# Optimization experiments

Hardware: AMD Instinct MI355X
Metric: run time of the kernel (lower is better)

## Reference

```python
import jax, jax.numpy as jnp
import numpy as np

THRESH = 0.5   # global `thresh` used by ActFun
LENS = 0.5     # global `lens` (surrogate width)
DECAY = 0.25   # LIFNode init_decay
INV_STD = 1.0 / float(np.sqrt(1.0 + 1e-5))  # BN eval: running_mean=0, running_var=1
HEADS = 8
WINDOW = 8

@jax.custom_vjp
def act_fun(x):
    return (x > THRESH).astype(x.dtype)

def _act_fwd(x):
    return act_fun(x), x

def _act_bwd(x, g):
    temp = (jnp.abs(x - THRESH) < LENS).astype(g.dtype) / (2.0 * LENS)
    return (g * temp,)

act_fun.defvjp(_act_fwd, _act_bwd)

def lif(x):
    # x: [T, ...]; mem = x[0]; mem_t = mem_{t-1}*decay*(1-spike_{t-1}.detach()) + x_t
    spike0 = act_fun(x[0])
    def step(carry, xi):
        mem_prev, spike_prev = carry
        mem = mem_prev * DECAY * (1.0 - jax.lax.stop_gradient(spike_prev)) + xi
        spike = act_fun(mem)
        return (mem, spike), spike
    _, spikes = jax.lax.scan(step, (x[0], spike0), x[1:])
    return jnp.concatenate([spike0[None], spikes], axis=0)

def bn_eval(x, gamma, beta):
    # BatchNorm2d eval over channel D (last dim of [T,B,L,D]) with default running stats
    return x * (INV_STD * gamma) + beta

def linear(x, w, b):
    # torch nn.Linear: y = x @ w.T + b, w: [out, in]
    return jnp.einsum('tbld,ed->tble', x, w) + b


def setup_inputs() -> dict:
    key = jax.random.key(0)
    ks = jax.random.split(key, 12)
    T, B, L, D = 4, 4, 1024, 512
    s = 0.02
    inp = {
        'x': jax.random.normal(ks[0], (T, B, L, D), dtype=jnp.float32),
        'pos_bias': jax.random.uniform(ks[1], (L, L), dtype=jnp.float32),
        'q_w': jax.random.normal(ks[2], (D, D), dtype=jnp.float32) * s,
        'q_b': jnp.zeros((D,), jnp.float32),
        'q_g': jnp.ones((D,), jnp.float32),
        'q_beta': jnp.zeros((D,), jnp.float32),
        'k_w': jax.random.normal(ks[3], (D, D), dtype=jnp.float32) * s,
        'k_b': jnp.zeros((D,), jnp.float32),
        'k_g': jnp.ones((D,), jnp.float32),
        'k_beta': jnp.zeros((D,), jnp.float32),
        'v_w': jax.random.normal(ks[4], (D, D), dtype=jnp.float32) * s,
        'v_b': jnp.zeros((D,), jnp.float32),
        'v_g': jnp.ones((D,), jnp.float32),
        'v_beta': jnp.zeros((D,), jnp.float32),
        'last_w': jax.random.normal(ks[5], (D, D), dtype=jnp.float32) * s,
        'last_b': jnp.zeros((D,), jnp.float32),
        'last_g': jnp.ones((D,), jnp.float32),
        'last_beta': jnp.zeros((D,), jnp.float32),
    }
    return inp


def reference(x, pos_bias, q_w, q_b, q_g, q_beta, k_w, k_b, k_g, k_beta,
              v_w, v_b, v_g, v_beta, last_w, last_b, last_g, last_beta):
    T, B, L, D = x.shape
    H = HEADS
    Dh = D // H
    # local causal band: keep pos_bias[i,j] only where 0 <= i-j < WINDOW
    i = jnp.arange(L)[:, None]
    j = jnp.arange(L)[None, :]
    band = ((i - j) >= 0) & ((i - j) < WINDOW)
    pb = jnp.where(band, pos_bias[:L, :L], 0.0)  # [L, L]

    xs = lif(x)  # first_lif
    q = lif(bn_eval(linear(xs, q_w, q_b), q_g, q_beta))
    k = lif(bn_eval(linear(xs, k_w, k_b), k_g, k_beta))
    v = lif(bn_eval(linear(xs, v_w, v_b), v_g, v_beta))

    # [T,B,L,D] -> [T,B,L,H,Dh] -> [B,H,L,T,Dh] -> [B,H,L,T*Dh]
    qh = q.reshape(T, B, L, H, Dh).transpose(1, 3, 2, 0, 4).reshape(B, H, L, T * Dh)
    kv = (k * v).reshape(T, B, L, H, Dh).transpose(1, 3, 2, 0, 4).reshape(B, H, L, T * Dh)

    attn = jnp.einsum('ij,bhjd->bhid', pb, kv)  # local-window positional mixing
    out = qh * attn
    out = out.reshape(B, H, L, T, Dh).transpose(3, 0, 2, 1, 4).reshape(T, B, L, D)
    out = lif(out)  # attn_lif
    out = bn_eval(linear(out, last_w, last_b), last_g, last_beta)
    return out
```

## Files before the change

### kernel.cpp

```cpp
#include <hip/hip_runtime.h>
#include <stdint.h>


#define T_ 4
#define B_ 4
#define L_ 1024
#define D_ 512
#define BI_ (B_*L_)
#define M_ROWS (T_*B_*L_)
#define STRIDE4 (B_*L_*D_/4)
#define INV_STD 0.9999950000374997f
#define EPS_FLAG 1e-3f
#define LIST_CAP 5000000u

typedef unsigned int   u32;
typedef unsigned short u16;
typedef __bf16 bf16x8 __attribute__((ext_vector_type(8)));
typedef float  f32x4  __attribute__((ext_vector_type(4)));

static __device__ __forceinline__ float spike_of(float m) {
  return m > 0.5f ? 1.0f : 0.0f;
}
static __device__ __forceinline__ u16 sbits(float s) {
  return s != 0.0f ? (u16)0x3F80 : (u16)0;
}

__device__ __forceinline__ void gll16(const u16* g, void* l) {
  __builtin_amdgcn_global_load_lds(
      (const __attribute__((address_space(1))) u32*)(const void*)g,
      (__attribute__((address_space(3))) u32*)l, 16, 0, 0);
}

__global__ __launch_bounds__(256) void k_wsplit(const float* __restrict__ qw,
    const float* __restrict__ kw, const float* __restrict__ vw,
    const float* __restrict__ lw, u16* __restrict__ wsp, u32* __restrict__ cnt) {
  int idx = blockIdx.x * 256 + threadIdx.x;
  if (idx == 0) *cnt = 0;
  int mat = idx >> 16;
  int u = idx & 65535;
  const float* W = mat == 0 ? qw : mat == 1 ? kw : mat == 2 ? vw : lw;
  float4 w = ((const float4*)W)[u];
  float wv[4] = {w.x, w.y, w.z, w.w};
  u16 hb[4], lb[4];
#pragma unroll
  for (int c = 0; c < 4; ++c) {
    __bf16 h = (__bf16)wv[c];
    float r = wv[c] - (float)h;
    __bf16 lo = (__bf16)r;
    hb[c] = __builtin_bit_cast(u16, h);
    lb[c] = __builtin_bit_cast(u16, lo);
  }
  u16* base = wsp + (size_t)mat * 524288;
  ((ushort4*)base)[u]            = make_ushort4(hb[0], hb[1], hb[2], hb[3]);
  ((ushort4*)(base + 262144))[u] = make_ushort4(lb[0], lb[1], lb[2], lb[3]);
}

__global__ __launch_bounds__(256) void k_lif_first(const float* __restrict__ x,
                                                   u16* __restrict__ xsb) {
  int idx = blockIdx.x * 256 + threadIdx.x;
  if (idx >= STRIDE4) return;
  const int bi = idx >> 7, d4 = idx & 127;
  const float4* x4 = (const float4*)x;
  ushort4* o4 = (ushort4*)xsb;
  float m[4], s[4];
  float4 v = x4[idx];
  m[0] = v.x; m[1] = v.y; m[2] = v.z; m[3] = v.w;
#pragma unroll
  for (int c = 0; c < 4; ++c) s[c] = spike_of(m[c]);
  o4[(bi * 4 + 0) * 128 + d4] =
      make_ushort4(sbits(s[0]), sbits(s[1]), sbits(s[2]), sbits(s[3]));
#pragma unroll
  for (int t = 1; t < T_; ++t) {
    v = x4[idx + t * STRIDE4];
    float xv[4] = {v.x, v.y, v.z, v.w};
#pragma unroll
    for (int c = 0; c < 4; ++c) {
      m[c] = m[c] * 0.25f * (1.0f - s[c]) + xv[c];
      s[c] = spike_of(m[c]);
    }
    o4[(bi * 4 + t) * 128 + d4] =
        make_ushort4(sbits(s[0]), sbits(s[1]), sbits(s[2]), sbits(s[3]));
  }
}

__device__ __forceinline__ void gemm_core(const u16* __restrict__ Ab,
    const u16* __restrict__ Wp, int row0, int col0, int tid,
    unsigned char* sm, f32x4 (&acc)[4][4]) {
  const u16* gsrc[12];
  int loff[12];
#pragma unroll
  for (int u = 0; u < 12; ++u) {
    if (u < 4) {
      int lin = u * 4096 + tid * 16;
      int r = lin >> 7, slot = (lin >> 4) & 7, gs = slot ^ (r & 7);
      gsrc[u] = Ab + (size_t)(row0 + r) * 512 + gs * 8;
      loff[u] = lin;
    } else {
      int lin = (u - 4) * 4096 + tid * 16;
      int plane = lin >> 14, l3 = lin & 16383;
      int r = l3 >> 7, slot = (l3 >> 4) & 7, gs = slot ^ (r & 7);
      gsrc[u] = Wp + (size_t)plane * 262144 + (size_t)(col0 + r) * 512 + gs * 8;
      loff[u] = 16384 + lin;
    }
  }
  const int lane = tid & 63;
  const int wid = tid >> 6;
  const int wr = wid >> 1, wc = wid & 1;
  const int la = lane & 15, lg = lane >> 4;

  int offA[4][2], offB[2][4][2];
#pragma unroll
  for (int mi = 0; mi < 4; ++mi) {
    int r = wr * 64 + mi * 16 + la;
#pragma unroll
    for (int s = 0; s < 2; ++s)
      offA[mi][s] = r * 128 + ((s * 64 + lg * 16) ^ ((r & 7) << 4));
  }
#pragma unroll
  for (int p = 0; p < 2; ++p)
#pragma unroll
    for (int ni = 0; ni < 4; ++ni) {
      int r = wc * 64 + ni * 16 + la;
#pragma unroll
      for (int s = 0; s < 2; ++s)
        offB[p][ni][s] = 16384 + p * 16384 + r * 128 +
                         ((s * 64 + lg * 16) ^ ((r & 7) << 4));
    }

#pragma unroll
  for (int a = 0; a < 4; ++a)
#pragma unroll
    for (int b = 0; b < 4; ++b) acc[a][b] = (f32x4){0.f, 0.f, 0.f, 0.f};

  for (int k0 = 0; k0 < 8; ++k0) {
#pragma unroll
    for (int u = 0; u < 12; ++u) gll16(gsrc[u] + (k0 << 6), sm + loff[u]);
    __syncthreads();
    uint4 af[4][2];
#pragma unroll
    for (int mi = 0; mi < 4; ++mi)
#pragma unroll
      for (int s = 0; s < 2; ++s)
        af[mi][s] = *(const uint4*)(sm + offA[mi][s]);
#pragma unroll
    for (int p = 0; p < 2; ++p)
#pragma unroll
      for (int s = 0; s < 2; ++s)
#pragma unroll
        for (int ni = 0; ni < 4; ++ni) {
          uint4 bf = *(const uint4*)(sm + offB[p][ni][s]);
#pragma unroll
          for (int mi = 0; mi < 4; ++mi)
            acc[mi][ni] = __builtin_amdgcn_mfma_f32_16x16x32_bf16(
                __builtin_bit_cast(bf16x8, af[mi][s]),
                __builtin_bit_cast(bf16x8, bf), acc[mi][ni], 0, 0, 0);
        }
    __syncthreads();
  }
}

__global__ __launch_bounds__(256) void k_gemm_qkv(const u16* __restrict__ Ab,
    const u16* __restrict__ wsp,
    const float* __restrict__ qb2, const float* __restrict__ qg,
    const float* __restrict__ qbe,
    const float* __restrict__ kb2, const float* __restrict__ kg,
    const float* __restrict__ kbe,
    const float* __restrict__ vb2, const float* __restrict__ vg,
    const float* __restrict__ vbe,
    u16* __restrict__ qs, u16* __restrict__ ks, u16* __restrict__ vs,
    u32* __restrict__ list, u32* __restrict__ cnt) {
  __shared__ __align__(16) unsigned char sm[49152];
  const int tid = threadIdx.x;
  const int tz = blockIdx.z;
  const u16* Wp = wsp + (size_t)tz * 524288;
  const float* Bb = tz == 0 ? qb2 : tz == 1 ? kb2 : vb2;
  const float* Gg = tz == 0 ? qg  : tz == 1 ? kg  : vg;
  const float* Be = tz == 0 ? qbe : tz == 1 ? kbe : vbe;
  u16* S          = tz == 0 ? qs  : tz == 1 ? ks  : vs;

  int f = blockIdx.y * 4 + blockIdx.x;
  int tI = (f & 7) * 64 + (f >> 3);
  const int row0 = (tI >> 2) * 128;
  const int col0 = (tI & 3) * 128;

  f32x4 acc[4][4];
  gemm_core(Ab, Wp, row0, col0, tid, sm, acc);

  const int lane = tid & 63;
  const int wid = tid >> 6;
  const int wr = wid >> 1, wc = wid & 1;
  const int la = lane & 15, lg = lane >> 4;

  u16* sm16 = (u16*)sm;
#pragma unroll
  for (int ni = 0; ni < 4; ++ni) {
    int cl = wc * 64 + ni * 16 + la;
    int e = col0 + cl;
    float cs = INV_STD * Gg[e];
    float cb = Bb[e], ct = Be[e];
#pragma unroll
    for (int mi = 0; mi < 4; ++mi) {
      int rl = wr * 64 + mi * 16 + lg * 4;
      int bi = (row0 + rl) >> 2;
      float m = 0.f, s = 0.f;
      int fl = 0;
#pragma unroll
      for (int p = 0; p < 4; ++p) {
        float pre = (acc[mi][ni][p] + cb) * cs + ct;
        if (p == 0) m = pre;
        else m = m * 0.25f * (1.0f - s) + pre;
        s = spike_of(m);
        if (fabsf(m - 0.5f) < EPS_FLAG) fl = 1;
        sm16[(rl + p) * 128 + cl] = sbits(s);
      }
      if (fl) {
        u32 pos = atomicAdd(cnt, 1u);
        if (pos < LIST_CAP)
          list[pos] = ((u32)tz << 21) | (u32)(bi * 512 + e);
      }
    }
  }
  __syncthreads();
#pragma unroll
  for (int ps = 0; ps < 8; ++ps) {
    int rr = ps * 16 + (tid >> 4);
    int c8 = (tid & 15) * 8;
    uint4 vv = *(const uint4*)(sm16 + rr * 128 + c8);
    *(uint4*)(S + (size_t)(row0 + rr) * 512 + col0 + c8) = vv;
  }
}

__global__ __launch_bounds__(256) void k_gemm_out(const u16* __restrict__ Ab,
    const u16* __restrict__ Wp, const float* __restrict__ bias,
    const float* __restrict__ gamma, const float* __restrict__ beta,
    float* __restrict__ Y) {
  __shared__ __align__(16) unsigned char sm[49152];
  const int tid = threadIdx.x;
  int f = blockIdx.y * 4 + blockIdx.x;
  int tI = (f & 7) * 64 + (f >> 3);
  const int row0 = (tI >> 2) * 128;
  const int col0 = (tI & 3) * 128;

  f32x4 acc[4][4];
  gemm_core(Ab, Wp, row0, col0, tid, sm, acc);

  const int lane = tid & 63;
  const int wid = tid >> 6;
  const int wr = wid >> 1, wc = wid & 1;
  const int la = lane & 15, lg = lane >> 4;

  float* sm32 = (float*)sm;
#pragma unroll
  for (int h = 0; h < 2; ++h) {
    if (wr == h) {
#pragma unroll
      for (int ni = 0; ni < 4; ++ni) {
        int cl = wc * 64 + ni * 16 + la;
        int e = col0 + cl;
        float cs = INV_STD * gamma[e];
        float cb = bias[e], ct = beta[e];
#pragma unroll
        for (int mi = 0; mi < 4; ++mi) {
          int rb = mi * 16 + lg * 4;
#pragma unroll
          for (int p = 0; p < 4; ++p)
            sm32[(rb + p) * 128 + cl] = (acc[mi][ni][p] + cb) * cs + ct;
        }
      }
    }
    __syncthreads();
    int rl = tid >> 2;
    int q0 = (tid & 3) * 32;
    int gr = row0 + h * 64 + rl;
    int bi = gr >> 2, p = gr & 3;
    float* dst = Y + ((size_t)p * BI_ + bi) * 512 + col0 + q0;
    const float* srcl = sm32 + rl * 128 + q0;
#pragma unroll
    for (int u = 0; u < 8; ++u)
      ((uint4*)dst)[u] = ((const uint4*)srcl)[u];
    __syncthreads();
  }
}

__device__ __forceinline__ void consume32_1(const float4 (&wb)[8],
                                            const uint4 (&ab)[4], float& c) {
#pragma unroll
  for (int u = 0; u < 8; ++u) {
    float4 w = wb[u];
    uint4 tt = ab[u >> 1];
    u32 a = (u & 1) ? tt.z : tt.x, b = (u & 1) ? tt.w : tt.y;
    c += (a & 0xFFFFu) ? w.x : 0.0f;
    c += (a >> 16)     ? w.y : 0.0f;
    c += (b & 0xFFFFu) ? w.z : 0.0f;
    c += (b >> 16)     ? w.w : 0.0f;
  }
}

__global__ __launch_bounds__(128) void k_fixup_c(const u16* __restrict__ xsb,
    u16* __restrict__ qs, u16* __restrict__ ks, u16* __restrict__ vs,
    const float* __restrict__ qw, const float* __restrict__ qb2,
    const float* __restrict__ qg, const float* __restrict__ qbe,
    const float* __restrict__ kw, const float* __restrict__ kb2,
    const float* __restrict__ kg, const float* __restrict__ kbe,
    const float* __restrict__ vw, const float* __restrict__ vb2,
    const float* __restrict__ vg, const float* __restrict__ vbe,
    const u32* __restrict__ list, const u32* __restrict__ cnt) {
  u32 n = *cnt;
  if (n > LIST_CAP) n = LIST_CAP;
  u32 tot = n * 4;
  for (u32 ii = blockIdx.x * 128 + threadIdx.x; ii < tot;
       ii += gridDim.x * 128) {
    u32 i = ii >> 2;
    int t = (int)(ii & 3);
    u32 e = list[i];
    int tz = (int)(e >> 21);
    int col = (int)(e & 0x1FFFFFu);
    int bi = col >> 9, d = col & 511;
    const float* W  = tz == 0 ? qw  : tz == 1 ? kw  : vw;
    const float* Bb = tz == 0 ? qb2 : tz == 1 ? kb2 : vb2;
    const float* Gg = tz == 0 ? qg  : tz == 1 ? kg  : vg;
    const float* Be = tz == 0 ? qbe : tz == 1 ? kbe : vbe;
    u16* S          = tz == 0 ? qs  : tz == 1 ? ks  : vs;
    const float4* w4 = (const float4*)(W + (size_t)d * 512);
    const uint4*  R  = (const uint4*)(xsb + ((size_t)bi * 4 + t) * 512);

    float4 wA[8], wB[8];
    uint4 aA[4], aB[4];
#pragma unroll
    for (int u = 0; u < 8; ++u) wA[u] = w4[u];
#pragma unroll
    for (int u = 0; u < 4; ++u) aA[u] = R[u];
    float c = 0.f;
#pragma unroll
    for (int ch = 0; ch < 16; ++ch) {
      if ((ch & 1) == 0) {
        if (ch + 1 < 16) {
          int wb0 = (ch + 1) * 8, ab0 = (ch + 1) * 4;
#pragma unroll
          for (int u = 0; u < 8; ++u) wB[u] = w4[wb0 + u];
#pragma unroll
          for (int u = 0; u < 4; ++u) aB[u] = R[ab0 + u];
        }
        consume32_1(wA, aA, c);
      } else {
        if (ch + 1 < 16) {
          int wb0 = (ch + 1) * 8, ab0 = (ch + 1) * 4;
#pragma unroll
          for (int u = 0; u < 8; ++u) wA[u] = w4[wb0 + u];
#pragma unroll
          for (int u = 0; u < 4; ++u) aA[u] = R[ab0 + u];
        }
        consume32_1(wB, aB, c);
      }
    }
    int lane = threadIdx.x & 63;
    int qb = lane & ~3;
    float cq[4];
    cq[0] = __shfl(c, qb + 0, 64);
    cq[1] = __shfl(c, qb + 1, 64);
    cq[2] = __shfl(c, qb + 2, 64);
    cq[3] = __shfl(c, qb + 3, 64);
    float cs = INV_STD * Gg[d];
    float cb = Bb[d], ct = Be[d];
    float m = 0.f, s = 0.f;
    u16 myb = 0;
#pragma unroll
    for (int t2 = 0; t2 < 4; ++t2) {
      float pre = (cq[t2] + cb) * cs + ct;
      if (t2 == 0) m = pre;
      else m = m * 0.25f * (1.0f - s) + pre;
      s = spike_of(m);
      if (t2 == t) myb = sbits(s);
    }
    S[((size_t)bi * 4 + t) * 512 + d] = myb;
  }
}

__global__ __launch_bounds__(256) void k_attn(const u16* __restrict__ qs,
    const u16* __restrict__ ks, const u16* __restrict__ vs,
    const float* __restrict__ pos_bias, u16* __restrict__ sout) {
  int idx = blockIdx.x * 256 + threadIdx.x;
  if (idx >= STRIDE4) return;
  const int d4 = idx & 127;
  const int bi = idx >> 7;
  const int i = bi & (L_ - 1);
  const int wmax = i < 7 ? i : 7;

  float pbv[8];
  const float* pbrow = pos_bias + (size_t)i * L_ + i;
  for (int w = 0; w <= wmax; ++w) pbv[w] = pbrow[-w];

  const ushort4* k4 = (const ushort4*)ks;
  const ushort4* v4 = (const ushort4*)vs;
  const ushort4* q4 = (const ushort4*)qs;
  float pre[T_][4];

#pragma unroll
  for (int t = 0; t < T_; ++t) {
    float sum[4] = {0.f, 0.f, 0.f, 0.f};
    for (int w = wmax; w >= 0; --w) {
      int rj = ((bi - w) * 4 + t) * 128 + d4;
      ushort4 ku = k4[rj];
      ushort4 vu = v4[rj];
      sum[0] += (ku.x && vu.x) ? pbv[w] : 0.0f;
      sum[1] += (ku.y && vu.y) ? pbv[w] : 0.0f;
      sum[2] += (ku.z && vu.z) ? pbv[w] : 0.0f;
      sum[3] += (ku.w && vu.w) ? pbv[w] : 0.0f;
    }
    ushort4 qu = q4[(bi * 4 + t) * 128 + d4];
    pre[t][0] = qu.x ? sum[0] : 0.0f;
    pre[t][1] = qu.y ? sum[1] : 0.0f;
    pre[t][2] = qu.z ? sum[2] : 0.0f;
    pre[t][3] = qu.w ? sum[3] : 0.0f;
  }

  ushort4* s4 = (ushort4*)sout;
  float m[4], s[4];
#pragma unroll
  for (int c = 0; c < 4; ++c) { m[c] = pre[0][c]; s[c] = spike_of(m[c]); }
  s4[(bi * 4 + 0) * 128 + d4] =
      make_ushort4(sbits(s[0]), sbits(s[1]), sbits(s[2]), sbits(s[3]));
#pragma unroll
  for (int t = 1; t < T_; ++t) {
#pragma unroll
    for (int c = 0; c < 4; ++c) {
      m[c] = m[c] * 0.25f * (1.0f - s[c]) + pre[t][c];
      s[c] = spike_of(m[c]);
    }
    s4[(bi * 4 + t) * 128 + d4] =
        make_ushort4(sbits(s[0]), sbits(s[1]), sbits(s[2]), sbits(s[3]));
  }
}

extern "C" void kernel_launch(void* const* d_in, const int* in_sizes, int n_in,
                              void* d_out, int out_size, void* d_ws, size_t ws_size,
                              hipStream_t stream) {
  (void)in_sizes; (void)n_in; (void)out_size; (void)ws_size;
  const float* x        = (const float*)d_in[0];
  const float* pos_bias = (const float*)d_in[1];
  const float* q_w    = (const float*)d_in[2];
  const float* q_b    = (const float*)d_in[3];
  const float* q_g    = (const float*)d_in[4];
  const float* q_beta = (const float*)d_in[5];
  const float* k_w    = (const float*)d_in[6];
  const float* k_b    = (const float*)d_in[7];
  const float* k_g    = (const float*)d_in[8];
  const float* k_beta = (const float*)d_in[9];
  const float* v_w    = (const float*)d_in[10];
  const float* v_b    = (const float*)d_in[11];
  const float* v_g    = (const float*)d_in[12];
  const float* v_beta = (const float*)d_in[13];
  const float* last_w    = (const float*)d_in[14];
  const float* last_b    = (const float*)d_in[15];
  const float* last_g    = (const float*)d_in[16];
  const float* last_beta = (const float*)d_in[17];
  float* out = (float*)d_out;

  char* ws = (char*)d_ws;
  u16*   xsb  = (u16*)(ws + 0);
  u16*   qs   = (u16*)(ws + 16777216);
  u16*   ks   = (u16*)(ws + 33554432);
  u16*   vs   = (u16*)(ws + 50331648);
  u16*   sA   = (u16*)(ws + 67108864);
  u16*   wsp  = (u16*)(ws + 100663296);
  u32*   list = (u32*)(ws + 104857600);
  u32*   cnt  = (u32*)(ws + 124857600);

  k_wsplit<<<1024, 256, 0, stream>>>(q_w, k_w, v_w, last_w, wsp, cnt);
  k_lif_first<<<2048, 256, 0, stream>>>(x, xsb);

  dim3 gq(4, 128, 3);
  k_gemm_qkv<<<gq, 256, 0, stream>>>(xsb, wsp,
      q_b, q_g, q_beta, k_b, k_g, k_beta, v_b, v_g, v_beta,
      qs, ks, vs, list, cnt);

  k_fixup_c<<<2048, 128, 0, stream>>>(xsb, qs, ks, vs,
      q_w, q_b, q_g, q_beta, k_w, k_b, k_g, k_beta, v_w, v_b, v_g, v_beta,
      list, cnt);

  k_attn<<<2048, 256, 0, stream>>>(qs, ks, vs, pos_bias, sA);

  dim3 gg(4, 128);
  k_gemm_out<<<gg, 256, 0, stream>>>(sA, wsp + 3 * 524288,
                                     last_b, last_g, last_beta, out);
}
```

Measured before the change: 348.6 us.

## Double-buffer GEMM K-tiles in LDS to overlap global loads with MFMA

```diff
diff --git a/kernel.cpp b/kernel.cpp
--- a/kernel.cpp
+++ b/kernel.cpp
@@ -86,45 +86,41 @@
 __device__ __forceinline__ void gemm_core(const u16* __restrict__ Ab,
     const u16* __restrict__ Wp, int row0, int col0, int tid,
     unsigned char* sm, f32x4 (&acc)[4][4]) {
-  const u16* gsrc[12];
-  int loff[12];
-#pragma unroll
-  for (int u = 0; u < 12; ++u) {
-    if (u < 4) {
-      int lin = u * 4096 + tid * 16;
-      int r = lin >> 7, slot = (lin >> 4) & 7, gs = slot ^ (r & 7);
-      gsrc[u] = Ab + (size_t)(row0 + r) * 512 + gs * 8;
-      loff[u] = lin;
-    } else {
-      int lin = (u - 4) * 4096 + tid * 16;
-      int plane = lin >> 14, l3 = lin & 16383;
-      int r = l3 >> 7, slot = (l3 >> 4) & 7, gs = slot ^ (r & 7);
-      gsrc[u] = Wp + (size_t)plane * 262144 + (size_t)(col0 + r) * 512 + gs * 8;
-      loff[u] = 16384 + lin;
-    }
-  }
   const int lane = tid & 63;
   const int wid = tid >> 6;
   const int wr = wid >> 1, wc = wid & 1;
   const int la = lane & 15, lg = lane >> 4;
 
-  int offA[4][2], offB[2][4][2];
+  const u16* gA[2]; int lA[2];
+#pragma unroll
+  for (int u = 0; u < 2; ++u) {
+    int lin = u * 4096 + tid * 16;
+    int r = lin >> 6, slot = (lin >> 4) & 3, gs = slot ^ (r & 3);
+    gA[u] = Ab + (size_t)(row0 + r) * 512 + gs * 8;
+    lA[u] = lin;
+  }
+  const u16* gB[4]; int lB[4];
+#pragma unroll
+  for (int u = 0; u < 4; ++u) {
+    int lin = u * 4096 + tid * 16;
+    int plane = lin >> 13, l2 = lin & 8191;
+    int r = l2 >> 6, slot = (l2 >> 4) & 3, gs = slot ^ (r & 3);
+    gB[u] = Wp + (size_t)plane * 262144 + (size_t)(col0 + r) * 512 + gs * 8;
+    lB[u] = 8192 + lin;
+  }
+
+  int offA[4], offB[2][4];
 #pragma unroll
   for (int mi = 0; mi < 4; ++mi) {
     int r = wr * 64 + mi * 16 + la;
-#pragma unroll
-    for (int s = 0; s < 2; ++s)
-      offA[mi][s] = r * 128 + ((s * 64 + lg * 16) ^ ((r & 7) << 4));
+    offA[mi] = r * 64 + ((lg ^ (r & 3)) << 4);
   }
 #pragma unroll
   for (int p = 0; p < 2; ++p)
 #pragma unroll
     for (int ni = 0; ni < 4; ++ni) {
       int r = wc * 64 + ni * 16 + la;
-#pragma unroll
-      for (int s = 0; s < 2; ++s)
-        offB[p][ni][s] = 16384 + p * 16384 + r * 128 +
-                         ((s * 64 + lg * 16) ^ ((r & 7) << 4));
+      offB[p][ni] = 8192 + p * 8192 + r * 64 + ((lg ^ (r & 3)) << 4);
     }
 
 #pragma unroll
@@ -132,29 +128,38 @@
 #pragma unroll
     for (int b = 0; b < 4; ++b) acc[a][b] = (f32x4){0.f, 0.f, 0.f, 0.f};
 
-  for (int k0 = 0; k0 < 8; ++k0) {
-#pragma unroll
-    for (int u = 0; u < 12; ++u) gll16(gsrc[u] + (k0 << 6), sm + loff[u]);
-    __syncthreads();
-    uint4 af[4][2];
-#pragma unroll
-    for (int mi = 0; mi < 4; ++mi)
-#pragma unroll
-      for (int s = 0; s < 2; ++s)
-        af[mi][s] = *(const uint4*)(sm + offA[mi][s]);
+#pragma unroll
+  for (int u = 0; u < 2; ++u) gll16(gA[u], sm + lA[u]);
+#pragma unroll
+  for (int u = 0; u < 4; ++u) gll16(gB[u], sm + lB[u]);
+  __syncthreads();
+
+#pragma unroll 2
+  for (int t = 0; t < 16; ++t) {
+    const int cur = t & 1;
+    const int nb = (cur ^ 1) * 24576;
+    if (t < 15) {
+      const int ko = (t + 1) * 32;
+#pragma unroll
+      for (int u = 0; u < 2; ++u) gll16(gA[u] + ko, sm + nb + lA[u]);
+#pragma unroll
+      for (int u = 0; u < 4; ++u) gll16(gB[u] + ko, sm + nb + lB[u]);
+    }
+    const unsigned char* bb = sm + cur * 24576;
+    uint4 af[4];
+#pragma unroll
+    for (int mi = 0; mi < 4; ++mi) af[mi] = *(const uint4*)(bb + offA[mi]);
 #pragma unroll
     for (int p = 0; p < 2; ++p)
 #pragma unroll
-      for (int s = 0; s < 2; ++s)
-#pragma unroll
-        for (int ni = 0; ni < 4; ++ni) {
-          uint4 bf = *(const uint4*)(sm + offB[p][ni][s]);
-#pragma unroll
-          for (int mi = 0; mi < 4; ++mi)
-            acc[mi][ni] = __builtin_amdgcn_mfma_f32_16x16x32_bf16(
-                __builtin_bit_cast(bf16x8, af[mi][s]),
-                __builtin_bit_cast(bf16x8, bf), acc[mi][ni], 0, 0, 0);
-        }
+      for (int ni = 0; ni < 4; ++ni) {
+        uint4 bf = *(const uint4*)(bb + offB[p][ni]);
+#pragma unroll
+        for (int mi = 0; mi < 4; ++mi)
+          acc[mi][ni] = __builtin_amdgcn_mfma_f32_16x16x32_bf16(
+              __builtin_bit_cast(bf16x8, af[mi]),
+              __builtin_bit_cast(bf16x8, bf), acc[mi][ni], 0, 0, 0);
+      }
     __syncthreads();
   }
 }
```

Result: no change. 355.5 us (+2.0%).

## Switch spike GEMMs to int8 MFMA with two-level per-row weight quantization

Applied to the files above, without the earlier changes.

```diff
diff --git a/kernel.cpp b/kernel.cpp
--- a/kernel.cpp
+++ b/kernel.cpp
@@ -7,68 +7,82 @@
 #define L_ 1024
 #define D_ 512
 #define BI_ (B_*L_)
-#define M_ROWS (T_*B_*L_)
 #define STRIDE4 (B_*L_*D_/4)
 #define INV_STD 0.9999950000374997f
 #define EPS_FLAG 1e-3f
 #define LIST_CAP 5000000u
 
 typedef unsigned int   u32;
-typedef unsigned short u16;
-typedef __bf16 bf16x8 __attribute__((ext_vector_type(8)));
-typedef float  f32x4  __attribute__((ext_vector_type(4)));
+typedef unsigned char  u8;
+typedef int i32x4 __attribute__((ext_vector_type(4)));
 
 static __device__ __forceinline__ float spike_of(float m) {
   return m > 0.5f ? 1.0f : 0.0f;
 }
-static __device__ __forceinline__ u16 sbits(float s) {
-  return s != 0.0f ? (u16)0x3F80 : (u16)0;
-}
-
-__device__ __forceinline__ void gll16(const u16* g, void* l) {
+
+__device__ __forceinline__ void gll16(const void* g, void* l) {
   __builtin_amdgcn_global_load_lds(
-      (const __attribute__((address_space(1))) u32*)(const void*)g,
+      (const __attribute__((address_space(1))) u32*)g,
       (__attribute__((address_space(3))) u32*)l, 16, 0, 0);
 }
 
 __global__ __launch_bounds__(256) void k_wsplit(const float* __restrict__ qw,
     const float* __restrict__ kw, const float* __restrict__ vw,
-    const float* __restrict__ lw, u16* __restrict__ wsp, u32* __restrict__ cnt) {
-  int idx = blockIdx.x * 256 + threadIdx.x;
-  if (idx == 0) *cnt = 0;
-  int mat = idx >> 16;
-  int u = idx & 65535;
+    const float* __restrict__ lw, u8* __restrict__ Wq,
+    float* __restrict__ scl, u32* __restrict__ cnt) {
+  if (blockIdx.x == 0 && threadIdx.x == 0) *cnt = 0;
+  int gid = blockIdx.x * 4 + (threadIdx.x >> 6);
+  int mat = gid >> 9, e = gid & 511;
+  int lane = threadIdx.x & 63;
   const float* W = mat == 0 ? qw : mat == 1 ? kw : mat == 2 ? vw : lw;
-  float4 w = ((const float4*)W)[u];
-  float wv[4] = {w.x, w.y, w.z, w.w};
-  u16 hb[4], lb[4];
-#pragma unroll
-  for (int c = 0; c < 4; ++c) {
-    __bf16 h = (__bf16)wv[c];
-    float r = wv[c] - (float)h;
-    __bf16 lo = (__bf16)r;
-    hb[c] = __builtin_bit_cast(u16, h);
-    lb[c] = __builtin_bit_cast(u16, lo);
-  }
-  u16* base = wsp + (size_t)mat * 524288;
-  ((ushort4*)base)[u]            = make_ushort4(hb[0], hb[1], hb[2], hb[3]);
-  ((ushort4*)(base + 262144))[u] = make_ushort4(lb[0], lb[1], lb[2], lb[3]);
+  const float4* w4 = (const float4*)(W + (size_t)e * 512 + lane * 8);
+  float4 wa = w4[0], wb = w4[1];
+  float w[8] = {wa.x, wa.y, wa.z, wa.w, wb.x, wb.y, wb.z, wb.w};
+  float am = 0.f;
+#pragma unroll
+  for (int j = 0; j < 8; ++j) am = fmaxf(am, fabsf(w[j]));
+#pragma unroll
+  for (int off = 1; off < 64; off <<= 1)
+    am = fmaxf(am, __shfl_xor(am, off, 64));
+  float s1 = am > 0.f ? am * (1.0f / 127.0f) : 1.0f;
+  float s2 = s1 * (1.0f / 254.0f);
+  float inv1 = 1.0f / s1, inv2 = 1.0f / s2;
+  u32 p1lo = 0, p1hi = 0, p2lo = 0, p2hi = 0;
+#pragma unroll
+  for (int j = 0; j < 8; ++j) {
+    float q1 = rintf(w[j] * inv1);
+    q1 = fminf(127.f, fmaxf(-127.f, q1));
+    float r = w[j] - s1 * q1;
+    float q2 = rintf(r * inv2);
+    q2 = fminf(127.f, fmaxf(-127.f, q2));
+    u32 b1 = (u32)(u8)(signed char)(int)q1;
+    u32 b2 = (u32)(u8)(signed char)(int)q2;
+    if (j < 4) { p1lo |= b1 << (j * 8); p2lo |= b2 << (j * 8); }
+    else       { p1hi |= b1 << ((j - 4) * 8); p2hi |= b2 << ((j - 4) * 8); }
+  }
+  u8* base = Wq + (size_t)mat * 524288 + (size_t)e * 512 + lane * 8;
+  *(uint2*)base             = make_uint2(p1lo, p1hi);
+  *(uint2*)(base + 262144)  = make_uint2(p2lo, p2hi);
+  if (lane == 0) {
+    scl[mat * 1024 + e] = s1;
+    scl[mat * 1024 + 512 + e] = s2;
+  }
 }
 
 __global__ __launch_bounds__(256) void k_lif_first(const float* __restrict__ x,
-                                                   u16* __restrict__ xsb) {
+                                                   u8* __restrict__ xsb) {
   int idx = blockIdx.x * 256 + threadIdx.x;
   if (idx >= STRIDE4) return;
   const int bi = idx >> 7, d4 = idx & 127;
   const float4* x4 = (const float4*)x;
-  ushort4* o4 = (ushort4*)xsb;
+  uchar4* o4 = (uchar4*)xsb;
   float m[4], s[4];
   float4 v = x4[idx];
   m[0] = v.x; m[1] = v.y; m[2] = v.z; m[3] = v.w;
 #pragma unroll
   for (int c = 0; c < 4; ++c) s[c] = spike_of(m[c]);
   o4[(bi * 4 + 0) * 128 + d4] =
-      make_ushort4(sbits(s[0]), sbits(s[1]), sbits(s[2]), sbits(s[3]));
+      make_uchar4((u8)s[0], (u8)s[1], (u8)s[2], (u8)s[3]);
 #pragma unroll
   for (int t = 1; t < T_; ++t) {
     v = x4[idx + t * STRIDE4];
@@ -79,27 +93,27 @@
       s[c] = spike_of(m[c]);
     }
     o4[(bi * 4 + t) * 128 + d4] =
-        make_ushort4(sbits(s[0]), sbits(s[1]), sbits(s[2]), sbits(s[3]));
-  }
-}
-
-__device__ __forceinline__ void gemm_core(const u16* __restrict__ Ab,
-    const u16* __restrict__ Wp, int row0, int col0, int tid,
-    unsigned char* sm, f32x4 (&acc)[4][4]) {
-  const u16* gsrc[12];
+        make_uchar4((u8)s[0], (u8)s[1], (u8)s[2], (u8)s[3]);
+  }
+}
+
+__device__ __forceinline__ void gemm_core_i8(const u8* __restrict__ Ab,
+    const u8* __restrict__ Wq2, int row0, int col0, int tid,
+    unsigned char* sm, i32x4 (&acc0)[4][4], i32x4 (&acc1)[4][4]) {
+  const u8* gsrc[12];
   int loff[12];
 #pragma unroll
   for (int u = 0; u < 12; ++u) {
     if (u < 4) {
       int lin = u * 4096 + tid * 16;
       int r = lin >> 7, slot = (lin >> 4) & 7, gs = slot ^ (r & 7);
-      gsrc[u] = Ab + (size_t)(row0 + r) * 512 + gs * 8;
+      gsrc[u] = Ab + (size_t)(row0 + r) * 512 + gs * 16;
       loff[u] = lin;
     } else {
       int lin = (u - 4) * 4096 + tid * 16;
       int plane = lin >> 14, l3 = lin & 16383;
       int r = l3 >> 7, slot = (l3 >> 4) & 7, gs = slot ^ (r & 7);
-      gsrc[u] = Wp + (size_t)plane * 262144 + (size_t)(col0 + r) * 512 + gs * 8;
+      gsrc[u] = Wq2 + (size_t)plane * 262144 + (size_t)(col0 + r) * 512 + gs * 16;
       loff[u] = 16384 + lin;
     }
   }
@@ -113,8 +127,8 @@
   for (int mi = 0; mi < 4; ++mi) {
     int r = wr * 64 + mi * 16 + la;
 #pragma unroll
-    for (int s = 0; s < 2; ++s)
-      offA[mi][s] = r * 128 + ((s * 64 + lg * 16) ^ ((r & 7) << 4));
+    for (int ks = 0; ks < 2; ++ks)
+      offA[mi][ks] = r * 128 + (((ks * 4 + lg) ^ (r & 7)) << 4);
   }
 #pragma unroll
   for (int p = 0; p < 2; ++p)
@@ -122,80 +136,94 @@
     for (int ni = 0; ni < 4; ++ni) {
       int r = wc * 64 + ni * 16 + la;
 #pragma unroll
-      for (int s = 0; s < 2; ++s)
-        offB[p][ni][s] = 16384 + p * 16384 + r * 128 +
-                         ((s * 64 + lg * 16) ^ ((r & 7) << 4));
+      for (int ks = 0; ks < 2; ++ks)
+        offB[p][ni][ks] = 16384 + p * 16384 + r * 128 +
+                          (((ks * 4 + lg) ^ (r & 7)) << 4);
     }
 
 #pragma unroll
   for (int a = 0; a < 4; ++a)
 #pragma unroll
-    for (int b = 0; b < 4; ++b) acc[a][b] = (f32x4){0.f, 0.f, 0.f, 0.f};
-
-  for (int k0 = 0; k0 < 8; ++k0) {
-#pragma unroll
-    for (int u = 0; u < 12; ++u) gll16(gsrc[u] + (k0 << 6), sm + loff[u]);
+    for (int b = 0; b < 4; ++b) {
+      acc0[a][b] = (i32x4){0, 0, 0, 0};
+      acc1[a][b] = (i32x4){0, 0, 0, 0};
+    }
+
+  for (int k0 = 0; k0 < 4; ++k0) {
+#pragma unroll
+    for (int u = 0; u < 12; ++u) gll16(gsrc[u] + (k0 << 7), sm + loff[u]);
     __syncthreads();
     uint4 af[4][2];
 #pragma unroll
     for (int mi = 0; mi < 4; ++mi)
 #pragma unroll
-      for (int s = 0; s < 2; ++s)
-        af[mi][s] = *(const uint4*)(sm + offA[mi][s]);
-#pragma unroll
-    for (int p = 0; p < 2; ++p)
-#pragma unroll
-      for (int s = 0; s < 2; ++s)
-#pragma unroll
-        for (int ni = 0; ni < 4; ++ni) {
-          uint4 bf = *(const uint4*)(sm + offB[p][ni][s]);
-#pragma unroll
-          for (int mi = 0; mi < 4; ++mi)
-            acc[mi][ni] = __builtin_amdgcn_mfma_f32_16x16x32_bf16(
-                __builtin_bit_cast(bf16x8, af[mi][s]),
-                __builtin_bit_cast(bf16x8, bf), acc[mi][ni], 0, 0, 0);
-        }
+      for (int ks = 0; ks < 2; ++ks)
+        af[mi][ks] = *(const uint4*)(sm + offA[mi][ks]);
+#pragma unroll
+    for (int ks = 0; ks < 2; ++ks)
+#pragma unroll
+      for (int ni = 0; ni < 4; ++ni) {
+        uint4 bf = *(const uint4*)(sm + offB[0][ni][ks]);
+#pragma unroll
+        for (int mi = 0; mi < 4; ++mi)
+          acc0[mi][ni] = __builtin_amdgcn_mfma_i32_16x16x64_i8(
+              __builtin_bit_cast(i32x4, af[mi][ks]),
+              __builtin_bit_cast(i32x4, bf), acc0[mi][ni], 0, 0, 0);
+      }
+#pragma unroll
+    for (int ks = 0; ks < 2; ++ks)
+#pragma unroll
+      for (int ni = 0; ni < 4; ++ni) {
+        uint4 bf = *(const uint4*)(sm + offB[1][ni][ks]);
+#pragma unroll
+        for (int mi = 0; mi < 4; ++mi)
+          acc1[mi][ni] = __builtin_amdgcn_mfma_i32_16x16x64_i8(
+              __builtin_bit_cast(i32x4, af[mi][ks]),
+              __builtin_bit_cast(i32x4, bf), acc1[mi][ni], 0, 0, 0);
+      }
     __syncthreads();
   }
 }
 
-__global__ __launch_bounds__(256) void k_gemm_qkv(const u16* __restrict__ Ab,
-    const u16* __restrict__ wsp,
+__global__ __launch_bounds__(256) void k_gemm_qkv(const u8* __restrict__ Ab,
+    const u8* __restrict__ Wq, const float* __restrict__ scl,
     const float* __restrict__ qb2, const float* __restrict__ qg,
     const float* __restrict__ qbe,
     const float* __restrict__ kb2, const float* __restrict__ kg,
     const float* __restrict__ kbe,
     const float* __restrict__ vb2, const float* __restrict__ vg,
     const float* __restrict__ vbe,
-    u16* __restrict__ qs, u16* __restrict__ ks, u16* __restrict__ vs,
+    u8* __restrict__ qs, u8* __restrict__ ks, u8* __restrict__ vs,
     u32* __restrict__ list, u32* __restrict__ cnt) {
   __shared__ __align__(16) unsigned char sm[49152];
   const int tid = threadIdx.x;
   const int tz = blockIdx.z;
-  const u16* Wp = wsp + (size_t)tz * 524288;
+  const u8* Wp = Wq + (size_t)tz * 524288;
   const float* Bb = tz == 0 ? qb2 : tz == 1 ? kb2 : vb2;
   const float* Gg = tz == 0 ? qg  : tz == 1 ? kg  : vg;
   const float* Be = tz == 0 ? qbe : tz == 1 ? kbe : vbe;
-  u16* S          = tz == 0 ? qs  : tz == 1 ? ks  : vs;
+  u8* S           = tz == 0 ? qs  : tz == 1 ? ks  : vs;
 
   int f = blockIdx.y * 4 + blockIdx.x;
   int tI = (f & 7) * 64 + (f >> 3);
   const int row0 = (tI >> 2) * 128;
   const int col0 = (tI & 3) * 128;
 
-  f32x4 acc[4][4];
-  gemm_core(Ab, Wp, row0, col0, tid, sm, acc);
+  i32x4 acc0[4][4], acc1[4][4];
+  gemm_core_i8(Ab, Wp, row0, col0, tid, sm, acc0, acc1);
 
   const int lane = tid & 63;
   const int wid = tid >> 6;
   const int wr = wid >> 1, wc = wid & 1;
   const int la = lane & 15, lg = lane >> 4;
 
-  u16* sm16 = (u16*)sm;
+  u8* sm8 = sm;
 #pragma unroll
   for (int ni = 0; ni < 4; ++ni) {
     int cl = wc * 64 + ni * 16 + la;
     int e = col0 + cl;
+    float s1 = scl[tz * 1024 + e];
+    float s2 = scl[tz * 1024 + 512 + e];
     float cs = INV_STD * Gg[e];
     float cb = Bb[e], ct = Be[e];
 #pragma unroll
@@ -206,12 +234,13 @@
       int fl = 0;
 #pragma unroll
       for (int p = 0; p < 4; ++p) {
-        float pre = (acc[mi][ni][p] + cb) * cs + ct;
+        float raw = s1 * (float)acc0[mi][ni][p] + s2 * (float)acc1[mi][ni][p];
+        float pre = (raw + cb) * cs + ct;
         if (p == 0) m = pre;
         else m = m * 0.25f * (1.0f - s) + pre;
         s = spike_of(m);
         if (fabsf(m - 0.5f) < EPS_FLAG) fl = 1;
-        sm16[(rl + p) * 128 + cl] = sbits(s);
+        sm8[(rl + p) * 128 + cl] = (u8)s;
       }
       if (fl) {
         u32 pos = atomicAdd(cnt, 1u);
@@ -222,18 +251,18 @@
   }
   __syncthreads();
 #pragma unroll
-  for (int ps = 0; ps < 8; ++ps) {
-    int rr = ps * 16 + (tid >> 4);
-    int c8 = (tid & 15) * 8;
-    uint4 vv = *(const uint4*)(sm16 + rr * 128 + c8);
-    *(uint4*)(S + (size_t)(row0 + rr) * 512 + col0 + c8) = vv;
-  }
-}
-
-__global__ __launch_bounds__(256) void k_gemm_out(const u16* __restrict__ Ab,
-    const u16* __restrict__ Wp, const float* __restrict__ bias,
-    const float* __restrict__ gamma, const float* __restrict__ beta,
-    float* __restrict__ Y) {
+  for (int ps = 0; ps < 4; ++ps) {
+    int rr = ps * 32 + (tid >> 3);
+    int c16 = (tid & 7) * 16;
+    uint4 vv = *(const uint4*)(sm8 + rr * 128 + c16);
+    *(uint4*)(S + (size_t)(row0 + rr) * 512 + col0 + c16) = vv;
+  }
+}
+
+__global__ __launch_bounds__(256) void k_gemm_out(const u8* __restrict__ Ab,
+    const u8* __restrict__ Wq, const float* __restrict__ scl,
+    const float* __restrict__ bias, const float* __restrict__ gamma,
+    const float* __restrict__ beta, float* __restrict__ Y) {
   __shared__ __align__(16) unsigned char sm[49152];
   const int tid = threadIdx.x;
   int f = blockIdx.y * 4 + blockIdx.x;
@@ -241,8 +270,8 @@
   const int row0 = (tI >> 2) * 128;
   const int col0 = (tI & 3) * 128;
 
-  f32x4 acc[4][4];
-  gemm_core(Ab, Wp, row0, col0, tid, sm, acc);
+  i32x4 acc0[4][4], acc1[4][4];
+  gemm_core_i8(Ab, Wq + 3 * 524288, row0, col0, tid, sm, acc0, acc1);
 
   const int lane = tid & 63;
   const int wid = tid >> 6;
@@ -257,14 +286,19 @@
       for (int ni = 0; ni < 4; ++ni) {
         int cl = wc * 64 + ni * 16 + la;
         int e = col0 + cl;
+        float s1 = scl[3 * 1024 + e];
+        float s2 = scl[3 * 1024 + 512 + e];
         float cs = INV_STD * gamma[e];
         float cb = bias[e], ct = beta[e];
 #pragma unroll
         for (int mi = 0; mi < 4; ++mi) {
           int rb = mi * 16 + lg * 4;
 #pragma unroll
-          for (int p = 0; p < 4; ++p)
-            sm32[(rb + p) * 128 + cl] = (acc[mi][ni][p] + cb) * cs + ct;
+          for (int p = 0; p < 4; ++p) {
+            float raw = s1 * (float)acc0[mi][ni][p] +
+                        s2 * (float)acc1[mi][ni][p];
+            sm32[(rb + p) * 128 + cl] = (raw + cb) * cs + ct;
+          }
         }
       }
     }
@@ -282,22 +316,23 @@
   }
 }
 
-__device__ __forceinline__ void consume32_1(const float4 (&wb)[8],
-                                            const uint4 (&ab)[4], float& c) {
+__device__ __forceinline__ void consume32_u8(const float4 (&wb)[8],
+                                             const uint4 (&ab)[2], float& c) {
 #pragma unroll
   for (int u = 0; u < 8; ++u) {
     float4 w = wb[u];
-    uint4 tt = ab[u >> 1];
-    u32 a = (u & 1) ? tt.z : tt.x, b = (u & 1) ? tt.w : tt.y;
-    c += (a & 0xFFFFu) ? w.x : 0.0f;
-    c += (a >> 16)     ? w.y : 0.0f;
-    c += (b & 0xFFFFu) ? w.z : 0.0f;
-    c += (b >> 16)     ? w.w : 0.0f;
-  }
-}
-
-__global__ __launch_bounds__(128) void k_fixup_c(const u16* __restrict__ xsb,
-    u16* __restrict__ qs, u16* __restrict__ ks, u16* __restrict__ vs,
+    uint4 t = ab[u >> 2];
+    u32 word = (u & 3) == 0 ? t.x : (u & 3) == 1 ? t.y
+             : (u & 3) == 2 ? t.z : t.w;
+    c += (word & 0xFFu)       ? w.x : 0.0f;
+    c += (word & 0xFF00u)     ? w.y : 0.0f;
+    c += (word & 0xFF0000u)   ? w.z : 0.0f;
+    c += (word >> 24)         ? w.w : 0.0f;
+  }
+}
+
+__global__ __launch_bounds__(128) void k_fixup_c(const u8* __restrict__ xsb,
+    u8* __restrict__ qs, u8* __restrict__ ks, u8* __restrict__ vs,
     const float* __restrict__ qw, const float* __restrict__ qb2,
     const float* __restrict__ qg, const float* __restrict__ qbe,
     const float* __restrict__ kw, const float* __restrict__ kb2,
@@ -320,37 +355,37 @@
     const float* Bb = tz == 0 ? qb2 : tz == 1 ? kb2 : vb2;
     const float* Gg = tz == 0 ? qg  : tz == 1 ? kg  : vg;
     const float* Be = tz == 0 ? qbe : tz == 1 ? kbe : vbe;
-    u16* S          = tz == 0 ? qs  : tz == 1 ? ks  : vs;
+    u8* S           = tz == 0 ? qs  : tz == 1 ? ks  : vs;
     const float4* w4 = (const float4*)(W + (size_t)d * 512);
     const uint4*  R  = (const uint4*)(xsb + ((size_t)bi * 4 + t) * 512);
 
     float4 wA[8], wB[8];
-    uint4 aA[4], aB[4];
+    uint4 aA[2], aB[2];
 #pragma unroll
     for (int u = 0; u < 8; ++u) wA[u] = w4[u];
 #pragma unroll
-    for (int u = 0; u < 4; ++u) aA[u] = R[u];
+    for (int u = 0; u < 2; ++u) aA[u] = R[u];
     float c = 0.f;
 #pragma unroll
     for (int ch = 0; ch < 16; ++ch) {
       if ((ch & 1) == 0) {
         if (ch + 1 < 16) {
-          int wb0 = (ch + 1) * 8, ab0 = (ch + 1) * 4;
+          int wb0 = (ch + 1) * 8, ab0 = (ch + 1) * 2;
 #pragma unroll
           for (int u = 0; u < 8; ++u) wB[u] = w4[wb0 + u];
 #pragma unroll
-          for (int u = 0; u < 4; ++u) aB[u] = R[ab0 + u];
+          for (int u = 0; u < 2; ++u) aB[u] = R[ab0 + u];
         }
-        consume32_1(wA, aA, c);
+        consume32_u8(wA, aA, c);
       } else {
         if (ch + 1 < 16) {
-          int wb0 = (ch + 1) * 8, ab0 = (ch + 1) * 4;
+          int wb0 = (ch + 1) * 8, ab0 = (ch + 1) * 2;
 #pragma unroll
           for (int u = 0; u < 8; ++u) wA[u] = w4[wb0 + u];
 #pragma unroll
-          for (int u = 0; u < 4; ++u) aA[u] = R[ab0 + u];
+          for (int u = 0; u < 2; ++u) aA[u] = R[ab0 + u];
         }
-        consume32_1(wB, aB, c);
+        consume32_u8(wB, aB, c);
       }
     }
     int lane = threadIdx.x & 63;
@@ -363,22 +398,22 @@
     float cs = INV_STD * Gg[d];
     float cb = Bb[d], ct = Be[d];
     float m = 0.f, s = 0.f;
-    u16 myb = 0;
+    u8 myb = 0;
 #pragma unroll
     for (int t2 = 0; t2 < 4; ++t2) {
       float pre = (cq[t2] + cb) * cs + ct;
       if (t2 == 0) m = pre;
       else m = m * 0.25f * (1.0f - s) + pre;
       s = spike_of(m);
-      if (t2 == t) myb = sbits(s);
+      if (t2 == t) myb = (u8)s;
     }
     S[((size_t)bi * 4 + t) * 512 + d] = myb;
   }
 }
 
-__global__ __launch_bounds__(256) void k_attn(const u16* __restrict__ qs,
-    const u16* __restrict__ ks, const u16* __restrict__ vs,
-    const float* __restrict__ pos_bias, u16* __restrict__ sout) {
+__global__ __launch_bounds__(256) void k_attn(const u8* __restrict__ qs,
+    const u8* __restrict__ ks, const u8* __restrict__ vs,
+    const float* __restrict__ pos_bias, u8* __restrict__ sout) {
   int idx = blockIdx.x * 256 + threadIdx.x;
   if (idx >= STRIDE4) return;
   const int d4 = idx & 127;
@@ -390,9 +425,9 @@
   const float* pbrow = pos_bias + (size_t)i * L_ + i;
   for (int w = 0; w <= wmax; ++w) pbv[w] = pbrow[-w];
 
-  const ushort4* k4 = (const ushort4*)ks;
-  const ushort4* v4 = (const ushort4*)vs;
-  const ushort4* q4 = (const ushort4*)qs;
+  const uchar4* k4 = (const uchar4*)ks;
+  const uchar4* v4 = (const uchar4*)vs;
+  const uchar4* q4 = (const uchar4*)qs;
   float pre[T_][4];
 
 #pragma unroll
@@ -400,26 +435,26 @@
     float sum[4] = {0.f, 0.f, 0.f, 0.f};
     for (int w = wmax; w >= 0; --w) {
       int rj = ((bi - w) * 4 + t) * 128 + d4;
-      ushort4 ku = k4[rj];
-      ushort4 vu = v4[rj];
+      uchar4 ku = k4[rj];
+      uchar4 vu = v4[rj];
       sum[0] += (ku.x && vu.x) ? pbv[w] : 0.0f;
       sum[1] += (ku.y && vu.y) ? pbv[w] : 0.0f;
       sum[2] += (ku.z && vu.z) ? pbv[w] : 0.0f;
       sum[3] += (ku.w && vu.w) ? pbv[w] : 0.0f;
     }
-    ushort4 qu = q4[(bi * 4 + t) * 128 + d4];
+    uchar4 qu = q4[(bi * 4 + t) * 128 + d4];
     pre[t][0] = qu.x ? sum[0] : 0.0f;
     pre[t][1] = qu.y ? sum[1] : 0.0f;
     pre[t][2] = qu.z ? sum[2] : 0.0f;
     pre[t][3] = qu.w ? sum[3] : 0.0f;
   }
 
-  ushort4* s4 = (ushort4*)sout;
+  uchar4* s4 = (uchar4*)sout;
   float m[4], s[4];
 #pragma unroll
   for (int c = 0; c < 4; ++c) { m[c] = pre[0][c]; s[c] = spike_of(m[c]); }
   s4[(bi * 4 + 0) * 128 + d4] =
-      make_ushort4(sbits(s[0]), sbits(s[1]), sbits(s[2]), sbits(s[3]));
+      make_uchar4((u8)s[0], (u8)s[1], (u8)s[2], (u8)s[3]);
 #pragma unroll
   for (int t = 1; t < T_; ++t) {
 #pragma unroll
@@ -428,7 +463,7 @@
       s[c] = spike_of(m[c]);
     }
     s4[(bi * 4 + t) * 128 + d4] =
-        make_ushort4(sbits(s[0]), sbits(s[1]), sbits(s[2]), sbits(s[3]));
+        make_uchar4((u8)s[0], (u8)s[1], (u8)s[2], (u8)s[3]);
   }
 }
 
@@ -457,20 +492,21 @@
   float* out = (float*)d_out;
 
   char* ws = (char*)d_ws;
-  u16*   xsb  = (u16*)(ws + 0);
-  u16*   qs   = (u16*)(ws + 16777216);
-  u16*   ks   = (u16*)(ws + 33554432);
-  u16*   vs   = (u16*)(ws + 50331648);
-  u16*   sA   = (u16*)(ws + 67108864);
-  u16*   wsp  = (u16*)(ws + 100663296);
-  u32*   list = (u32*)(ws + 104857600);
-  u32*   cnt  = (u32*)(ws + 124857600);
-
-  k_wsplit<<<1024, 256, 0, stream>>>(q_w, k_w, v_w, last_w, wsp, cnt);
+  u8*    xsb  = (u8*)(ws + 0);
+  u8*    qs   = (u8*)(ws + 8388608);
+  u8*    ks   = (u8*)(ws + 16777216);
+  u8*    vs   = (u8*)(ws + 25165824);
+  u8*    sA   = (u8*)(ws + 33554432);
+  u8*    Wq   = (u8*)(ws + 41943040);
+  float* scl  = (float*)(ws + 46137344);
+  u32*   list = (u32*)(ws + 50331648);
+  u32*   cnt  = (u32*)(ws + 73400320);
+
+  k_wsplit<<<512, 256, 0, stream>>>(q_w, k_w, v_w, last_w, Wq, scl, cnt);
   k_lif_first<<<2048, 256, 0, stream>>>(x, xsb);
 
   dim3 gq(4, 128, 3);
-  k_gemm_qkv<<<gq, 256, 0, stream>>>(xsb, wsp,
+  k_gemm_qkv<<<gq, 256, 0, stream>>>(xsb, Wq, scl,
       q_b, q_g, q_beta, k_b, k_g, k_beta, v_b, v_g, v_beta,
       qs, ks, vs, list, cnt);
 
@@ -481,6 +517,6 @@
   k_attn<<<2048, 256, 0, stream>>>(qs, ks, vs, pos_bias, sA);
 
   dim3 gg(4, 128);
-  k_gemm_out<<<gg, 256, 0, stream>>>(sA, wsp + 3 * 524288,
+  k_gemm_out<<<gg, 256, 0, stream>>>(sA, Wq, scl,
                                      last_b, last_g, last_beta, out);
 }
```

After: 330.4 us. 1.06x faster.
